# Kernel tuning notes

Hardware: AMD Instinct MI355X
Metric: run time of the kernel (lower is better)

The kernel has to match this reference:

```python
import jax, jax.numpy as jnp
import numpy as np

PATCH = 3  # patch_size, padding = PATCH//2 = 1, stride = 1
EPS = 1e-12  # F.normalize eps


def extract_patches(x):
    """F.unfold(k=3, stride=1, pad=1) then reshape to [B, N, C, 3, 3] (N=H*W)."""
    b, c, h, w = x.shape
    xp = jnp.pad(x, ((0, 0), (0, 0), (1, 1), (1, 1)))
    # stack the 9 shifted views: [B, C, 9, H, W]; order (kh, kw) matches torch unfold
    shifts = [xp[:, :, i:i + h, j:j + w] for i in range(PATCH) for j in range(PATCH)]
    p = jnp.stack(shifts, axis=2)
    p = p.reshape(b, c, PATCH, PATCH, h * w)
    return jnp.transpose(p, (0, 4, 1, 2, 3))  # [B, N, C, 3, 3]


def cosine_similarity(x, y):
    """x, y: [B, N, ...] patch sets -> [B, Nx, Ny] cosine similarity."""
    b = x.shape[0]
    xf = x.reshape(b, x.shape[1], -1)
    yf = y.reshape(b, y.shape[1], -1)
    xn = xf / jnp.maximum(jnp.linalg.norm(xf, axis=2, keepdims=True), EPS)
    yn = yf / jnp.maximum(jnp.linalg.norm(yf, axis=2, keepdims=True), EPS)
    return jnp.einsum('bnd,bmd->bnm', xn, yn)


def setup_inputs() -> dict:
    key = jax.random.key(0)
    k1, k2, k3, k4 = jax.random.split(key, 4)
    B, C, H, W = 2, 64, 80, 80
    return {
        'content_feat': jax.random.normal(k1, (B, C, H, W), dtype=jnp.float32),
        'style_feat': jax.random.normal(k2, (B, C, H, W), dtype=jnp.float32),
        'content_mask': jax.random.uniform(k3, (B, 3, H, W), dtype=jnp.float32),
        'style_mask': jax.random.uniform(k4, (B, 3, H, W), dtype=jnp.float32),
    }


def reference(content_feat, style_feat, content_mask, style_mask):
    content_patches = extract_patches(content_feat)      # [B, N, C, 3, 3]
    style_patches = extract_patches(style_feat)          # [B, N, C, 3, 3]
    cmask_patches = extract_patches(content_mask)        # [B, N, 3, 3, 3]
    smask_patches = extract_patches(style_mask)          # [B, N, 3, 3, 3]

    feat_sim = cosine_similarity(content_patches, style_patches)   # [B, N, N]
    mask_sim = cosine_similarity(cmask_patches, smask_patches)     # [B, N, N]
    similarity = feat_sim * mask_sim

    best = jnp.argmax(similarity, axis=2)                # [B, N]
    b, n = best.shape
    sp_flat = style_patches.reshape(b, n, -1)            # [B, N, C*9]
    matched = jnp.take_along_axis(sp_flat, best[:, :, None], axis=1)
    return matched.reshape(style_patches.shape)          # [B, N, C, 3, 3]
```

## Files before the change

### kernel.cpp

```cpp
#include <hip/hip_runtime.h>

#define HH 80
#define WW 80
#define NPIX 6400
#define PW 82
#define NPP (PW*PW)
#define CFE 64
#define CMA 3
#define KF 576
#define GUARD 1024
#define NREG 8

#define PA 1024
#define POUT 856
#define BW 1056

typedef unsigned long long u64;
typedef unsigned int u32;

__device__ __forceinline__ void gload4(const float* g, float* l) {
    __builtin_amdgcn_global_load_lds((const __attribute__((address_space(1))) void*)g,
                                     (__attribute__((address_space(3))) void*)l, 4, 0, 0);
}
__device__ __forceinline__ float4 ld4(const float* p) { return *(const float4*)p; }

__global__ __launch_bounds__(256)
void pixsq_kernel(const float* __restrict__ sf, const float* __restrict__ sm,
                  float* __restrict__ psf, float* __restrict__ psm) {
    int g = blockIdx.x * 256 + threadIdx.x;
    if (g >= 2 * NPIX) return;
    int b = g / NPIX, m = g - b * NPIX;
    const float* p = sf + (size_t)b * CFE * NPIX + m;
    float a = 0.f;
    #pragma unroll 8
    for (int c = 0; c < CFE; ++c) { float v = p[c * NPIX]; a = fmaf(v, v, a); }
    const float* q = sm + (size_t)b * CMA * NPIX + m;
    float am = 0.f;
    #pragma unroll
    for (int c = 0; c < CMA; ++c) { float v = q[c * NPIX]; am = fmaf(v, v, am); }
    psf[g] = a; psm[g] = am;
}

__global__ __launch_bounds__(256)
void rn2_kernel(const float* __restrict__ psf, const float* __restrict__ psm,
                float* __restrict__ rn2p) {
    int g = blockIdx.x * 256 + threadIdx.x;
    if (g >= 2 * NPIX) return;
    int b = g / NPIX, m = g - b * NPIX;
    int mh = m / WW, mw = m - mh * WW;
    float sF = 0.f, sM = 0.f;
    #pragma unroll
    for (int di = -1; di <= 1; ++di) {
        if ((unsigned)(mh + di) >= HH) continue;
        #pragma unroll
        for (int dj = -1; dj <= 1; ++dj) {
            if ((unsigned)(mw + dj) >= WW) continue;
            int mm = m + di * WW + dj;
            sF += psf[b * NPIX + mm];
            sM += psm[b * NPIX + mm];
        }
    }
    float rf = 1.f / fmaxf(sqrtf(sF), 1e-12f);
    float rm = 1.f / fmaxf(sqrtf(sM), 1e-12f);
    rn2p[(size_t)b * NPP + (mh + 1) * PW + (mw + 1)] = rf * rm;
}

__global__ __launch_bounds__(256)
void pad_kernel(const float* __restrict__ cf, const float* __restrict__ sf,
                const float* __restrict__ cm, const float* __restrict__ sm,
                float* __restrict__ cfp, float* __restrict__ sfp,
                float* __restrict__ cmp, float* __restrict__ smp) {
    int gid = blockIdx.x * 256 + threadIdx.x;
    if (gid >= 2 * 2 * 67 * NPIX) return;
    int pix = gid % NPIX; int t = gid / NPIX;
    int c = t % 67; t /= 67;
    int b = t & 1; int which = t >> 1;
    int h = pix / WW, w = pix - h * WW;
    int qq = (h + 1) * PW + (w + 1);
    if (which == 0) {
        if (c < 64) cfp[((size_t)b * CFE + c) * NPP + qq] = cf[((size_t)b * CFE + c) * NPIX + pix];
        else        cmp[((size_t)b * CMA + (c - 64)) * NPP + qq] = cm[((size_t)b * CMA + (c - 64)) * NPIX + pix];
    } else {
        if (c < 64) sfp[((size_t)b * CFE + c) * NPP + qq] = sf[((size_t)b * CFE + c) * NPIX + pix];
        else        smp[((size_t)b * CMA + (c - 64)) * NPP + qq] = sm[((size_t)b * CMA + (c - 64)) * NPIX + pix];
    }
}

__global__ __launch_bounds__(1024, 4)
void fuse_kernel(const float* __restrict__ cfp, const float* __restrict__ sfp,
                 const float* __restrict__ cmp, const float* __restrict__ smp,
                 const float* __restrict__ rn2p, u64* __restrict__ pbest) {
    const int pt = blockIdx.y;
    const int b  = blockIdx.z;
    const int pstart = 83 + POUT * pt;
    const int pend   = min(pstart + POUT, 6641);
    const int pbase  = pstart - 84;
    const int dte0   = (6644 - pend) >> 5;
    const int dtemax = (13200 - pstart) >> 5;
    const int dte = dte0 + blockIdx.x;
    if (dte > dtemax) return;
    const int d0 = -6560 + 32 * dte;

    __shared__ float pool[PA * 36];

    const int tid = threadIdx.x;
    const int tp = tid & 255;
    const int tg = tid >> 8;
    const int wb = tid & 960;
    const int swz = (((tp & 7) ^ ((tp >> 3) & 7)) << 2);

    const float* cfb = cfp + (size_t)b * CFE * NPP + pbase;
    const float* sfb = sfp + (size_t)b * CFE * NPP + pbase + d0;
    const float* cmb = cmp + (size_t)b * CMA * NPP + pbase;
    const float* smb = smp + (size_t)b * CMA * NPP + pbase + d0;

    float acc[4][8];
    float pdM[8][4];

    auto zacc = [&]() {
        #pragma unroll
        for (int k = 0; k < 4; ++k)
            #pragma unroll
            for (int j = 0; j < 8; ++j) acc[k][j] = 0.f;
    };

    auto stageF = [&](int q, int buf) {
        float* Ab = pool + buf * 16640;
        float* Bb = Ab + 8 * PA;
        const float* As = cfb + (size_t)(q * 8) * NPP;
        const float* Bs = sfb + (size_t)(q * 8) * NPP;
        #pragma unroll
        for (int cc = 0; cc < 8; ++cc) {
            gload4(As + cc * NPP + tid, Ab + cc * PA + wb);
            gload4(Bs + cc * NPP + tid, Bb + cc * BW + wb);
            if (tid < 32) gload4(Bs + cc * NPP + 1024 + tid, Bb + cc * BW + 1024);
        }
    };

    auto gemmc = [&](const float* Ab, const float* Bb) {
        const float* Ar = Ab + 4 * tp;
        const float* Br = Bb + 4 * tp + 8 * tg;
        float a[4], bb[12];
        *(float4*)a        = ld4(Ar);
        *(float4*)bb       = ld4(Br);
        *(float4*)(bb + 4) = ld4(Br + 4);
        *(float4*)(bb + 8) = ld4(Br + 8);
        #pragma unroll
        for (int k = 0; k < 4; ++k)
            #pragma unroll
            for (int j = 0; j < 8; ++j)
                acc[k][j] = fmaf(a[k], bb[k + j], acc[k][j]);
    };

    auto s0write = [&]() {
        #pragma unroll
        for (int k = 0; k < 4; ++k) {
            float* dr = pool + (4 * tp + k) * 36;
            *(float4*)(dr + ((8 * tg) ^ swz)) =
                make_float4(acc[k][0], acc[k][1], acc[k][2], acc[k][3]);
            *(float4*)(dr + ((8 * tg + 4) ^ swz)) =
                make_float4(acc[k][4], acc[k][5], acc[k][6], acc[k][7]);
        }
    };

    #define RD(rr) ld4(pool + (rr) * 36 + ((4 * dg) ^ (((((rr) >> 2) & 7) ^ (((rr) >> 5) & 7)) << 2)))

    #pragma unroll
    for (int cc = 0; cc < 3; ++cc) {
        gload4(cmb + cc * NPP + tid, pool + cc * PA + wb);
        gload4(smb + cc * NPP + tid, pool + 3 * PA + cc * BW + wb);
        if (tid < 32) gload4(smb + cc * NPP + 1024 + tid, pool + 3 * PA + cc * BW + 1024);
    }
    __syncthreads();
    zacc();
    #pragma unroll
    for (int cc = 0; cc < 3; ++cc)
        gemmc(pool + cc * PA, pool + 3 * PA + cc * BW);
    __syncthreads();
    s0write();
    __syncthreads();

    if (tid < 856) {
        const int rg = tid >> 3, dg = tid & 7;
        const int p0w = 84 + 8 * rg;
        #pragma unroll
        for (int k = 0; k < 8; ++k)
            #pragma unroll
            for (int j = 0; j < 4; ++j) pdM[k][j] = 0.f;
        static const int dg3[3] = {-82, 0, 82};
        #pragma unroll
        for (int g = 0; g < 3; ++g) {
            const int rb0 = p0w + dg3[g] - 1;
            float4 c0 = RD(rb0);
            float4 c1 = RD(rb0 + 1);
            #pragma unroll
            for (int k = 0; k < 8; ++k) {
                float4 c2 = RD(rb0 + 2 + k);
                pdM[k][0] += c0.x + c1.x + c2.x;
                pdM[k][1] += c0.y + c1.y + c2.y;
                pdM[k][2] += c0.z + c1.z + c2.z;
                pdM[k][3] += c0.w + c1.w + c2.w;
                c0 = c1; c1 = c2;
            }
        }
    }
    __syncthreads();

    zacc();
    stageF(0, 0);
    __syncthreads();
    #pragma unroll 1
    for (int q = 0; q < 8; ++q) {
        const int buf = q & 1;
        if (q < 7) stageF(q + 1, buf ^ 1);
        const float* Ab = pool + buf * 16640;
        const float* Bb = Ab + 8 * PA;
        #pragma unroll 2
        for (int cc = 0; cc < 8; ++cc)
            gemmc(Ab + cc * PA, Bb + cc * BW);
        __syncthreads();
    }
    s0write();
    __syncthreads();

    if (tid < 856) {
        const int rg = tid >> 3, dg = tid & 7;
        const int p0w = 84 + 8 * rg;
        const int ra = p0w - 83, rbw = p0w - 1, rc = p0w + 81;
        const float* rnb = rn2p + (size_t)b * NPP;
        u64* pb = pbest + ((size_t)(dte & (NREG - 1)) * 2 + b) * NPIX;

        float4 wa0 = RD(ra),      wa1 = RD(ra + 1);
        float4 wb0 = RD(rbw),     wb1 = RD(rbw + 1);
        float4 wc0 = RD(rc),      wc1 = RD(rc + 1);
        #pragma unroll
        for (int k = 0; k < 8; ++k) {
            float4 wa2 = RD(ra + 2 + k);
            float4 wb2 = RD(rbw + 2 + k);
            float4 wc2 = RD(rc + 2 + k);
            float f0 = wa0.x + wa1.x + wa2.x + wb0.x + wb1.x + wb2.x + wc0.x + wc1.x + wc2.x;
            float f1 = wa0.y + wa1.y + wa2.y + wb0.y + wb1.y + wb2.y + wc0.y + wc1.y + wc2.y;
            float f2 = wa0.z + wa1.z + wa2.z + wb0.z + wb1.z + wb2.z + wc0.z + wc1.z + wc2.z;
            float f3 = wa0.w + wa1.w + wa2.w + wb0.w + wb1.w + wb2.w + wc0.w + wc1.w + wc2.w;
            wa0 = wa1; wa1 = wa2; wb0 = wb1; wb1 = wb2; wc0 = wc1; wc1 = wc2;

            const int row = p0w + k;
            const int p = pbase + row;
            const int ph = p / PW, pw2 = p - ph * PW;
            const bool ok = (p < pend) && (ph >= 1) && (ph <= 80) && (pw2 >= 1) && (pw2 <= 80);
            u64 key = 0;
            if (ok) {
                float pf[4] = {f0, f1, f2, f3};
                #pragma unroll
                for (int j = 0; j < 4; ++j) {
                    int mp = p + d0 + 4 * dg + j;
                    if ((unsigned)mp >= (unsigned)NPP) continue;
                    float r2 = rnb[mp];
                    if (r2 == 0.f) continue;
                    float sc = pf[j] * pdM[k][j] * r2;
                    sc += 0.f;
                    u32 u = __float_as_uint(sc);
                    u ^= (u >> 31) ? 0xFFFFFFFFu : 0x80000000u;
                    u64 k2 = ((u64)u << 32) | (u32)~(u32)mp;
                    if (k2 > key) key = k2;
                }
            }
            u64 o;
            o = __shfl_xor(key, 1); if (o > key) key = o;
            o = __shfl_xor(key, 2); if (o > key) key = o;
            o = __shfl_xor(key, 4); if (o > key) key = o;
            if (dg == 0 && key) {
                const int n_real = (ph - 1) * 80 + (pw2 - 1);
                u64 cur = pb[n_real];
                if (key > cur) atomicMax(&pb[n_real], key);
            }
        }
    }
    #undef RD
}

__global__ __launch_bounds__(64)
void gather_kernel(const float* __restrict__ sf, const u64* __restrict__ pbest,
                   float* __restrict__ out) {
    int n = blockIdx.x, b = blockIdx.y;
    int lane = threadIdx.x;

    u64 key = 0;
    #pragma unroll
    for (int r = 0; r < NREG; ++r) {
        u64 k = pbest[((size_t)r * 2 + b) * NPIX + n];
        if (k > key) key = k;
    }
    int mp = (int)(~(u32)key);
    int m = 0;
    if ((unsigned)mp < (unsigned)NPP) {
        int ph = mp / PW, pw = mp - ph * PW;
        if (ph >= 1 && ph <= 80 && pw >= 1 && pw <= 80)
            m = (ph - 1) * 80 + (pw - 1);
    }
    int mh = m / WW, mw = m - mh * WW;
    const float* sfb = sf + (size_t)b * CFE * NPIX;
    float* ob = out + ((size_t)b * NPIX + n) * (size_t)KF;
    #pragma unroll
    for (int e = lane; e < KF; e += 64) {
        int c = e / 9, pos = e - c * 9;
        int di = pos / 3 - 1, dj = pos - (pos / 3) * 3 - 1;
        int h = mh + di, w = mw + dj;
        ob[e] = ((unsigned)h < HH && (unsigned)w < WW) ? sfb[c * NPIX + h * WW + w] : 0.f;
    }
}

extern "C" void kernel_launch(void* const* d_in, const int* in_sizes, int n_in,
                              void* d_out, int out_size, void* d_ws, size_t ws_size,
                              hipStream_t stream) {
    const float* cf = (const float*)d_in[0];
    const float* sf = (const float*)d_in[1];
    const float* cm = (const float*)d_in[2];
    const float* sm = (const float*)d_in[3];
    float* out = (float*)d_out;

    float* psf = (float*)d_ws;
    float* psm = psf + 2 * NPIX;
    u64*  pbest = (u64*)(psm + 2 * NPIX);
    float* rn2p = (float*)(pbest + (size_t)NREG * 2 * NPIX);
    float* padreg = rn2p + 2 * NPP;
    float* cfp = padreg + GUARD;
    float* sfp = cfp + (size_t)2 * CFE * NPP + GUARD;
    float* cmp = sfp + (size_t)2 * CFE * NPP + GUARD;
    float* smp = cmp + (size_t)2 * CMA * NPP + GUARD;

    size_t zero_bytes = (size_t)NREG * 2 * NPIX * 8 +
        ((size_t)2 * NPP + (size_t)5 * GUARD +
         (size_t)4 * CFE * NPP + (size_t)4 * CMA * NPP) * 4;
    hipMemsetAsync(pbest, 0, zero_bytes, stream);

    pad_kernel<<<(2 * 2 * 67 * NPIX + 255) / 256, 256, 0, stream>>>(
        cf, sf, cm, sm, cfp, sfp, cmp, smp);
    pixsq_kernel<<<(2 * NPIX + 255) / 256, 256, 0, stream>>>(sf, sm, psf, psm);
    rn2_kernel  <<<(2 * NPIX + 255) / 256, 256, 0, stream>>>(psf, psm, rn2p);

    fuse_kernel<<<dim3(232, 8, 2), 1024, 0, stream>>>(cfp, sfp, cmp, smp, rn2p, pbest);

    gather_kernel<<<dim3(NPIX, 2), 64, 0, stream>>>(sf, pbest, out);
}
```

Baseline: 633.8 us.

## Halve fuse tile to 512 threads and load A operand directly from global

The fused similarity kernel's pixel tile shrinks from 1024 to 512 threads (POUT 344, more y-tiles). The content-side A operand is no longer staged in LDS; each thread reads its float4 of A straight from global memory into registers, and only B is double-buffered in shared memory. This cuts LDS footprint and traffic per block, which should allow more resident blocks. The cost is more redundant B halo loads, because the tiles are smaller and more numerous, and global latency on A reads that are no longer covered by the async LDS prefetch.

```diff
diff --git a/kernel.cpp b/kernel.cpp
--- a/kernel.cpp
+++ b/kernel.cpp
@@ -11,12 +11,14 @@
 #define GUARD 1024
 #define NREG 8
 
-#define PA 1024
-#define POUT 856
-#define BW 1056
+#define PA 512
+#define POUT 344
+#define BW 544
 
 typedef unsigned long long u64;
 typedef unsigned int u32;
+
+struct f4u { float x, y, z, w; };
 
 __device__ __forceinline__ void gload4(const float* g, float* l) {
     __builtin_amdgcn_global_load_lds((const __attribute__((address_space(1))) void*)g,
@@ -86,7 +88,7 @@
     }
 }
 
-__global__ __launch_bounds__(1024, 4)
+__global__ __launch_bounds__(512, 4)
 void fuse_kernel(const float* __restrict__ cfp, const float* __restrict__ sfp,
                  const float* __restrict__ cmp, const float* __restrict__ smp,
                  const float* __restrict__ rn2p, u64* __restrict__ pbest) {
@@ -104,15 +106,15 @@
     __shared__ float pool[PA * 36];
 
     const int tid = threadIdx.x;
-    const int tp = tid & 255;
-    const int tg = tid >> 8;
-    const int wb = tid & 960;
+    const int tp = tid & 127;
+    const int tg = tid >> 7;
+    const int wb = tid & 448;
     const int swz = (((tp & 7) ^ ((tp >> 3) & 7)) << 2);
 
-    const float* cfb = cfp + (size_t)b * CFE * NPP + pbase;
-    const float* sfb = sfp + (size_t)b * CFE * NPP + pbase + d0;
-    const float* cmb = cmp + (size_t)b * CMA * NPP + pbase;
-    const float* smb = smp + (size_t)b * CMA * NPP + pbase + d0;
+    const float* Ag  = cfp + (size_t)b * CFE * NPP + pbase + 4 * tp;
+    const float* Bg  = sfp + (size_t)b * CFE * NPP + pbase + d0;
+    const float* AgM = cmp + (size_t)b * CMA * NPP + pbase + 4 * tp;
+    const float* BgM = smp + (size_t)b * CMA * NPP + pbase + d0;
 
     float acc[4][8];
     float pdM[8][4];
@@ -124,27 +126,23 @@
             for (int j = 0; j < 8; ++j) acc[k][j] = 0.f;
     };
 
-    auto stageF = [&](int q, int buf) {
-        float* Ab = pool + buf * 16640;
-        float* Bb = Ab + 8 * PA;
-        const float* As = cfb + (size_t)(q * 8) * NPP;
-        const float* Bs = sfb + (size_t)(q * 8) * NPP;
+    auto stageB = [&](int q, int buf) {
+        float* Bb = pool + buf * (8 * BW);
+        const float* Bs = Bg + (size_t)(q * 8) * NPP;
         #pragma unroll
         for (int cc = 0; cc < 8; ++cc) {
-            gload4(As + cc * NPP + tid, Ab + cc * PA + wb);
             gload4(Bs + cc * NPP + tid, Bb + cc * BW + wb);
-            if (tid < 32) gload4(Bs + cc * NPP + 1024 + tid, Bb + cc * BW + 1024);
+            if (tid < 32) gload4(Bs + cc * NPP + 512 + tid, Bb + cc * BW + 512);
         }
     };
 
-    auto gemmc = [&](const float* Ab, const float* Bb) {
-        const float* Ar = Ab + 4 * tp;
+    auto gemmc1 = [&](const f4u& a4, const float* Bb) {
         const float* Br = Bb + 4 * tp + 8 * tg;
-        float a[4], bb[12];
-        *(float4*)a        = ld4(Ar);
+        float bb[12];
         *(float4*)bb       = ld4(Br);
         *(float4*)(bb + 4) = ld4(Br + 4);
         *(float4*)(bb + 8) = ld4(Br + 8);
+        const float a[4] = {a4.x, a4.y, a4.z, a4.w};
         #pragma unroll
         for (int k = 0; k < 4; ++k)
             #pragma unroll
@@ -165,22 +163,26 @@
 
     #define RD(rr) ld4(pool + (rr) * 36 + ((4 * dg) ^ (((((rr) >> 2) & 7) ^ (((rr) >> 5) & 7)) << 2)))
 
-    #pragma unroll
-    for (int cc = 0; cc < 3; ++cc) {
-        gload4(cmb + cc * NPP + tid, pool + cc * PA + wb);
-        gload4(smb + cc * NPP + tid, pool + 3 * PA + cc * BW + wb);
-        if (tid < 32) gload4(smb + cc * NPP + 1024 + tid, pool + 3 * PA + cc * BW + 1024);
-    }
-    __syncthreads();
-    zacc();
-    #pragma unroll
-    for (int cc = 0; cc < 3; ++cc)
-        gemmc(pool + cc * PA, pool + 3 * PA + cc * BW);
+    {
+        f4u Am0 = *(const f4u*)(AgM);
+        f4u Am1 = *(const f4u*)(AgM + (size_t)NPP);
+        f4u Am2 = *(const f4u*)(AgM + (size_t)2 * NPP);
+        #pragma unroll
+        for (int cc = 0; cc < 3; ++cc) {
+            gload4(BgM + (size_t)cc * NPP + tid, pool + cc * BW + wb);
+            if (tid < 32) gload4(BgM + (size_t)cc * NPP + 512 + tid, pool + cc * BW + 512);
+        }
+        __syncthreads();
+        zacc();
+        gemmc1(Am0, pool);
+        gemmc1(Am1, pool + BW);
+        gemmc1(Am2, pool + 2 * BW);
+    }
     __syncthreads();
     s0write();
     __syncthreads();
 
-    if (tid < 856) {
+    if (tid < 344) {
         const int rg = tid >> 3, dg = tid & 7;
         const int p0w = 84 + 8 * rg;
         #pragma unroll
@@ -207,32 +209,38 @@
     __syncthreads();
 
     zacc();
-    stageF(0, 0);
+    stageB(0, 0);
     __syncthreads();
     #pragma unroll 1
     for (int q = 0; q < 8; ++q) {
         const int buf = q & 1;
-        if (q < 7) stageF(q + 1, buf ^ 1);
-        const float* Ab = pool + buf * 16640;
-        const float* Bb = Ab + 8 * PA;
-        #pragma unroll 2
-        for (int cc = 0; cc < 8; ++cc)
-            gemmc(Ab + cc * PA, Bb + cc * BW);
+        if (q < 7) stageB(q + 1, buf ^ 1);
+        const float* Bb = pool + buf * (8 * BW);
+        #pragma unroll
+        for (int half = 0; half < 2; ++half) {
+            f4u A0[4];
+            #pragma unroll
+            for (int c = 0; c < 4; ++c)
+                A0[c] = *(const f4u*)(Ag + (size_t)(q * 8 + half * 4 + c) * NPP);
+            #pragma unroll
+            for (int c = 0; c < 4; ++c)
+                gemmc1(A0[c], Bb + (half * 4 + c) * BW);
+        }
         __syncthreads();
     }
     s0write();
     __syncthreads();
 
-    if (tid < 856) {
+    if (tid < 344) {
         const int rg = tid >> 3, dg = tid & 7;
         const int p0w = 84 + 8 * rg;
         const int ra = p0w - 83, rbw = p0w - 1, rc = p0w + 81;
         const float* rnb = rn2p + (size_t)b * NPP;
         u64* pb = pbest + ((size_t)(dte & (NREG - 1)) * 2 + b) * NPIX;
 
-        float4 wa0 = RD(ra),      wa1 = RD(ra + 1);
-        float4 wb0 = RD(rbw),     wb1 = RD(rbw + 1);
-        float4 wc0 = RD(rc),      wc1 = RD(rc + 1);
+        float4 wa0 = RD(ra),  wa1 = RD(ra + 1);
+        float4 wb0 = RD(rbw), wb1 = RD(rbw + 1);
+        float4 wc0 = RD(rc),  wc1 = RD(rc + 1);
         #pragma unroll
         for (int k = 0; k < 8; ++k) {
             float4 wa2 = RD(ra + 2 + k);
@@ -339,7 +347,7 @@
     pixsq_kernel<<<(2 * NPIX + 255) / 256, 256, 0, stream>>>(sf, sm, psf, psm);
     rn2_kernel  <<<(2 * NPIX + 255) / 256, 256, 0, stream>>>(psf, psm, rn2p);
 
-    fuse_kernel<<<dim3(232, 8, 2), 1024, 0, stream>>>(cfp, sfp, cmp, smp, rn2p, pbest);
+    fuse_kernel<<<dim3(217, 20, 2), 512, 0, stream>>>(cfp, sfp, cmp, smp, rn2p, pbest);
 
     gather_kernel<<<dim3(NPIX, 2), 64, 0, stream>>>(sf, pbest, out);
 }
```

After: 903.4 us. +42.5%, slower.
